# Kernel tuning notes

Measured on AMD Instinct MI355X. Metric: run time of the kernel, lower is better.

Reference implementation:

```python
import jax, jax.numpy as jnp
import numpy as np

D_MODEL = 1024
D_STATE = 64
D_CONV = 4
EXPAND = 2
HEADDIM = 64
NGROUPS = 1
D_INNER = EXPAND * D_MODEL          # 2048 (= d_ssm)
NHEADS = D_INNER // HEADDIM         # 32
CONV_DIM = D_INNER + 2 * NGROUPS * D_STATE      # 2176
D_IN_PROJ = 2 * D_INNER + 2 * NGROUPS * D_STATE + NHEADS  # 4256
BATCH, SEQLEN = 1, 1024
EPS = 1e-5


def silu(x):
    return x * jax.nn.sigmoid(x)


def _causal_dwconv(xBC, conv_w, conv_b):
    # xBC: (B, L, C); conv_w: (C, W) depthwise; causal padding W-1 on the left
    x = jnp.transpose(xBC, (0, 2, 1))  # (B, C, L)
    y = jax.lax.conv_general_dilated(
        x, conv_w[:, None, :], window_strides=(1,),
        padding=[(conv_w.shape[-1] - 1, 0)],
        feature_group_count=x.shape[1])
    return jnp.transpose(y, (0, 2, 1)) + conv_b


def _mamba_dir(u, W_in, conv_w, conv_b, dt_bias, A_log, D, norm_w, W_out):
    B, L, _ = u.shape
    H, P, G, N = NHEADS, HEADDIM, NGROUPS, D_STATE
    zxbcdt = u @ W_in.T                               # (B, L, D_IN_PROJ)
    z = zxbcdt[..., :D_INNER]
    xBC = zxbcdt[..., D_INNER:D_INNER + CONV_DIM]
    dt = zxbcdt[..., -H:]
    xBC = silu(_causal_dwconv(xBC, conv_w, conv_b))
    x = xBC[..., :D_INNER].reshape(B, L, H, P)
    Bm = xBC[..., D_INNER:D_INNER + G * N].reshape(B, L, G, N)
    Cm = xBC[..., D_INNER + G * N:].reshape(B, L, G, N)
    dt = jax.nn.softplus(dt + dt_bias)                # (B, L, H)
    A = -jnp.exp(A_log.astype(jnp.float32))           # (H,)
    rep = H // G
    Bh = jnp.repeat(Bm, rep, axis=2)                  # (B, L, H, N)
    Ch = jnp.repeat(Cm, rep, axis=2)
    dA = jnp.exp(dt * A)                              # (B, L, H)
    dtx = dt[..., None] * x                           # (B, L, H, P)

    def step(h, inp):
        dA_t, dtx_t, Bh_t, Ch_t = inp                 # (B,H), (B,H,P), (B,H,N), (B,H,N)
        h = h * dA_t[..., None, None] + jnp.einsum('bhp,bhn->bhpn', dtx_t, Bh_t)
        y = jnp.einsum('bhpn,bhn->bhp', h, Ch_t)
        return h, y

    h0 = jnp.zeros((B, H, P, N), dtype=u.dtype)
    inputs = (dA.swapaxes(0, 1), dtx.swapaxes(0, 1),
              Bh.swapaxes(0, 1), Ch.swapaxes(0, 1))
    _, ys = jax.lax.scan(step, h0, inputs)            # ys: (L, B, H, P)
    y = ys.swapaxes(0, 1) + D[None, None, :, None] * x
    y = y.reshape(B, L, D_INNER)
    # gated RMSNorm (norm_before_gate=False): norm(y * silu(z)), group = d_ssm/ngroups
    yg = y * silu(z)
    yg = yg.reshape(B, L, G, -1)
    yg = yg * jax.lax.rsqrt(jnp.mean(yg * yg, axis=-1, keepdims=True) + EPS)
    yg = yg.reshape(B, L, D_INNER) * norm_w
    return yg @ W_out.T                               # (B, L, d_model)


def _forward(u, W_in_f, W_in_b, conv_w_f, conv_b_f, conv_w_b, conv_b_b,
             dt_bias_f, dt_bias_b, A_log_f, A_log_b, D_f, D_b,
             norm_w_f, norm_w_b, W_out_f, W_out_b, W_out):
    out_f = _mamba_dir(u, W_in_f, conv_w_f, conv_b_f, dt_bias_f, A_log_f,
                       D_f, norm_w_f, W_out_f)
    ub = jnp.flip(u, axis=1)
    out_b = _mamba_dir(ub, W_in_b, conv_w_b, conv_b_b, dt_bias_b, A_log_b,
                       D_b, norm_w_b, W_out_b)
    out = silu(jnp.concatenate([out_f, jnp.flip(out_b, axis=1)], axis=-1))
    return out @ W_out.T


def setup_inputs() -> dict:
    key = jax.random.key(0)
    ks = jax.random.split(key, 20)
    s = 0.02

    def dt_init(k):
        dt = jnp.exp(jax.random.uniform(k, (NHEADS,)) *
                     (np.log(0.1) - np.log(0.001)) + np.log(0.001))
        return dt + jnp.log(-jnp.expm1(-dt))  # inverse softplus

    def a_init(k):
        return jnp.log(jax.random.uniform(k, (NHEADS,), minval=1.0, maxval=16.0))

    return {
        'u': jax.random.normal(ks[0], (BATCH, SEQLEN, D_MODEL), jnp.float32),
        'W_in_f': jax.random.normal(ks[1], (D_IN_PROJ, D_MODEL), jnp.float32) * s,
        'W_in_b': jax.random.normal(ks[2], (D_IN_PROJ, D_MODEL), jnp.float32) * s,
        'conv_w_f': jax.random.normal(ks[3], (CONV_DIM, D_CONV), jnp.float32) * 0.2,
        'conv_b_f': jnp.zeros((CONV_DIM,), jnp.float32),
        'conv_w_b': jax.random.normal(ks[4], (CONV_DIM, D_CONV), jnp.float32) * 0.2,
        'conv_b_b': jnp.zeros((CONV_DIM,), jnp.float32),
        'dt_bias_f': dt_init(ks[5]),
        'dt_bias_b': dt_init(ks[6]),
        'A_log_f': a_init(ks[7]),
        'A_log_b': a_init(ks[8]),
        'D_f': jnp.ones((NHEADS,), jnp.float32),
        'D_b': jnp.ones((NHEADS,), jnp.float32),
        'norm_w_f': jnp.ones((D_INNER,), jnp.float32),
        'norm_w_b': jnp.ones((D_INNER,), jnp.float32),
        'W_out_f': jax.random.normal(ks[9], (D_MODEL, D_INNER), jnp.float32) * s,
        'W_out_b': jax.random.normal(ks[10], (D_MODEL, D_INNER), jnp.float32) * s,
        'W_out': jax.random.normal(ks[11], (D_MODEL, 2 * D_MODEL), jnp.float32) * s,
    }


def reference(u, W_in_f, W_in_b, conv_w_f, conv_b_f, conv_w_b, conv_b_b,
              dt_bias_f, dt_bias_b, A_log_f, A_log_b, D_f, D_b,
              norm_w_f, norm_w_b, W_out_f, W_out_b, W_out):
    return _forward(u, W_in_f, W_in_b, conv_w_f, conv_b_f, conv_w_b, conv_b_b,
                    dt_bias_f, dt_bias_b, A_log_f, A_log_b, D_f, D_b,
                    norm_w_f, norm_w_b, W_out_f, W_out_b, W_out)
```

## Files before the change

### kernel.cpp

```cpp
#include <hip/hip_runtime.h>
#include <hip/hip_bf16.h>
#include <stdint.h>

#define LSEQ   1024
#define DINNER 2048
#define CONVD  2176
#define LDP    4352
#define NH     32
#define HD     64
#define NST    64
#define CHUNK  64
#define NCH    16
#define LDT    72

#define POFF_CWF  0
#define POFF_CBF  8704
#define POFF_CWB  10880
#define POFF_CBB  19584
#define POFF_DTBF 21760
#define POFF_DTBB 21792
#define POFF_ALF  21824
#define POFF_ALB  21856
#define POFF_DF   21888
#define POFF_DB   21920
#define POFF_NWF  21952
#define POFF_NWB  24000
#define PTOT      26048

#define BF16_ONES 0x3F803F80u

typedef short v8s __attribute__((ext_vector_type(8)));
typedef short v4s __attribute__((ext_vector_type(4)));
typedef float v4f __attribute__((ext_vector_type(4)));
using bf16 = __hip_bfloat16;

__device__ __forceinline__ float loadf(const void* p, size_t i, int isbf) {
    return isbf ? __bfloat162float(((const bf16*)p)[i]) : ((const float*)p)[i];
}
__device__ __forceinline__ float s2f(short s) {
    unsigned u = ((unsigned)(unsigned short)s) << 16; float f;
    __builtin_memcpy(&f, &u, 4); return f;
}
__device__ __forceinline__ short f2s(float f) {
    bf16 b = __float2bfloat16(f); short s;
    __builtin_memcpy(&s, &b, 2); return s;
}
__device__ __forceinline__ void load8(const void* p, size_t i, int isbf, float* o) {
    if (isbf) {
        v8s s = *(const v8s*)((const short*)p + i);
        #pragma unroll
        for (int e = 0; e < 8; e++) o[e] = s2f(s[e]);
    } else {
        float4 a = *(const float4*)((const float*)p + i);
        float4 b = *(const float4*)((const float*)p + i + 4);
        o[0] = a.x; o[1] = a.y; o[2] = a.z; o[3] = a.w;
        o[4] = b.x; o[5] = b.y; o[6] = b.z; o[7] = b.w;
    }
}
__device__ __forceinline__ v8s pack8(const float* o) {
    v8s r;
    #pragma unroll
    for (int e = 0; e < 8; e++) r[e] = f2s(o[e]);
    return r;
}

__device__ __forceinline__ void gload16(const bf16* g, bf16* l) {
    __builtin_amdgcn_global_load_lds(
        (const __attribute__((address_space(1))) void*)g,
        (__attribute__((address_space(3))) void*)l, 16, 0, 0);
}

template<int V> __device__ __forceinline__ void vwait() {
    if constexpr (V == 0) asm volatile("s_waitcnt vmcnt(0)" ::: "memory");
    else if constexpr (V == 3) asm volatile("s_waitcnt vmcnt(3)" ::: "memory");
    else if constexpr (V == 4) asm volatile("s_waitcnt vmcnt(4)" ::: "memory");
    else if constexpr (V == 6) asm volatile("s_waitcnt vmcnt(6)" ::: "memory");
    else if constexpr (V == 8) asm volatile("s_waitcnt vmcnt(8)" ::: "memory");
}

#define NPU  262144
#define NPW  1114112
#define NWO  786432
#define NSEG (NPU + NPW + NWO)
__global__ void prep_all(const void* __restrict__ U, const void* __restrict__ Wf, const void* __restrict__ Wb,
                         const void* __restrict__ Wof, const void* __restrict__ Wob, const void* __restrict__ Wom,
                         const void* cwf, const void* cbf, const void* cwb, const void* cbb,
                         const void* dtbf, const void* dtbb, const void* alf, const void* alb,
                         const void* df, const void* db, const void* nwf, const void* nwb,
                         bf16* __restrict__ Au, bf16* __restrict__ Wp,
                         bf16* __restrict__ Woc, bf16* __restrict__ Wo2,
                         float* __restrict__ P, int* __restrict__ flag)
{
    int idx = blockIdx.x * 256 + threadIdx.x;
    int f = (((const unsigned int*)nwf)[0] == BF16_ONES) ? 1 : 0;
    if (idx < NPU) {
        int r = idx >> 7, c8 = (idx & 127) * 8;
        int src = (r < 1024) ? r : (2047 - r);
        float o[8]; load8(U, (size_t)src * 1024 + c8, f, o);
        *(v8s*)(Au + (size_t)r * 1024 + c8) = pack8(o);
    } else if (idx < NPU + NPW) {
        int j = idx - NPU;
        int r = (j >> 7) % 4352;
        int d = j / (4352 * 128);
        int c8 = (j & 127) * 8;
        float o[8] = {0.f, 0.f, 0.f, 0.f, 0.f, 0.f, 0.f, 0.f};
        if (r < 4256) load8(d ? Wb : Wf, (size_t)r * 1024 + c8, f, o);
        *(v8s*)(Wp + (size_t)j * 8) = pack8(o);
    } else if (idx < NSEG) {
        int j = idx - NPU - NPW;
        int seg = j / 262144;
        size_t j8 = (size_t)(j % 262144) * 8;
        float o[8];
        if (seg == 0)      { load8(Wof, j8, f, o); *(v8s*)(Woc + j8) = pack8(o); }
        else if (seg == 1) { load8(Wob, j8, f, o); *(v8s*)(Woc + 1024 * 2048 + j8) = pack8(o); }
        else               { load8(Wom, j8, f, o); *(v8s*)(Wo2 + j8) = pack8(o); }
    } else if (idx < NSEG + PTOT) {
        int j = idx - NSEG;
        if (j == 0) *flag = f;
        float v;
        if      (j < POFF_CBF)  v = loadf(cwf,  j,              f);
        else if (j < POFF_CWB)  v = loadf(cbf,  j - POFF_CBF,   f);
        else if (j < POFF_CBB)  v = loadf(cwb,  j - POFF_CWB,   f);
        else if (j < POFF_DTBF) v = loadf(cbb,  j - POFF_CBB,   f);
        else if (j < POFF_DTBB) v = loadf(dtbf, j - POFF_DTBF,  f);
        else if (j < POFF_ALF)  v = loadf(dtbb, j - POFF_DTBB,  f);
        else if (j < POFF_ALB)  v = loadf(alf,  j - POFF_ALF,   f);
        else if (j < POFF_DF)   v = loadf(alb,  j - POFF_ALB,   f);
        else if (j < POFF_DB)   v = loadf(df,   j - POFF_DF,    f);
        else if (j < POFF_NWF)  v = loadf(db,   j - POFF_DB,    f);
        else if (j < POFF_NWB)  v = loadf(nwf,  j - POFF_NWF,   f);
        else                    v = loadf(nwb,  j - POFF_NWB,   f);
        P[j] = v;
    }
}

template<int BM, int BN, int BK>
__global__ __launch_bounds__(256) void gemm_bt(
    const bf16* __restrict__ A, const bf16* __restrict__ B0, const bf16* __restrict__ B1,
    int rowSplit, void* __restrict__ Cv, int M, int N, int K, const int* outFlag,
    int epi, int swzMode)
{
    constexpr int RPL = 2048 / BK;
    constexpr int AN  = BM / RPL;
    constexpr int BNN = BN / RPL;
    constexpr int LPS = AN + BNN;
    constexpr int MI  = BM / 32;
    constexpr int NJ  = BN / 32;
    constexpr int KS  = BK / 32;
    constexpr int CPR = BK / 8;
    __shared__ __align__(16) bf16 LdsA[4][BM * BK];
    __shared__ __align__(16) bf16 LdsB[4][BN * BK];
    const int tid  = threadIdx.x;
    const int lane = tid & 63;
    const int wave = tid >> 6;
    const int quad = lane >> 4, l16 = lane & 15;
    const int wrow = (wave >> 1) * (BM / 2);
    const int wcol = (wave & 1)  * (BN / 2);

    int bx = blockIdx.x, by = blockIdx.y;
    if (swzMode >= 0) {
        const int gx = gridDim.x, gy = gridDim.y;
        const int nwg = gx * gy;
        const int cpx = nwg >> 3;
        const int p   = by * gx + bx;
        const int L   = (p & 7) * cpx + (p >> 3);
        if (swzMode) { by = L % gy; bx = L / gy; }
        else         { bx = L % gx; by = L / gx; }
    }
    const int m0 = by * BM;
    const int n0 = bx * BN;
    const bf16* Bp = (m0 >= rowSplit) ? B1 : B0;
    const int mode = (outFlag && !epi) ? *outFlag : 1;

    const int r0 = tid / CPR;
    const int pc = tid % CPR;
    const int fx_w = (BK == 32) ? ((r0 >> 1) & 3) : (r0 & 7);
    const int csw = (pc ^ fx_w) * 8;
    const bf16* gA[AN];
    const bf16* gB[BNN];
    #pragma unroll
    for (int a = 0; a < AN; a++)  gA[a] = A  + (size_t)(m0 + r0 + RPL * a) * K + csw;
    #pragma unroll
    for (int q = 0; q < BNN; q++) gB[q] = Bp + (size_t)(n0 + r0 + RPL * q) * K + csw;

    v4f acc[MI][NJ];
    #pragma unroll
    for (int i = 0; i < MI; i++)
        #pragma unroll
        for (int j = 0; j < NJ; j++) acc[i][j] = (v4f){0.f, 0.f, 0.f, 0.f};

    const int nt = K / BK;

    auto STAGE = [&](int buf, int t) {
        const int k0 = t * BK;
        #pragma unroll
        for (int a = 0; a < AN; a++)
            gload16(gA[a] + k0, &LdsA[buf][a * 2048 + tid * 8]);
        #pragma unroll
        for (int q = 0; q < BNN; q++)
            gload16(gB[q] + k0, &LdsB[buf][q * 2048 + tid * 8]);
    };

    STAGE(0, 0);
    STAGE(1, 1);
    STAGE(2, 2);

    for (int t = 0; t < nt; ++t) {
        const int buf = t & 3;
        if (t < nt - 2)       vwait<2 * LPS>();
        else if (t == nt - 2) vwait<LPS>();
        else                  vwait<0>();
        __builtin_amdgcn_s_barrier();
        if (t + 3 < nt) STAGE((t + 3) & 3, t + 3);

        const bf16* as = &LdsA[buf][0];
        const bf16* bs = &LdsB[buf][0];
        #pragma unroll
        for (int ks = 0; ks < KS; ks++) {
            v8s af[MI], bfr[NJ];
            #pragma unroll
            for (int i = 0; i < MI; i++) {
                int row = wrow + i * 16 + l16;
                int fx = (BK == 32) ? ((row >> 1) & 3) : (row & 7);
                af[i] = *(const v8s*)&as[row * BK + (((ks * 4 + quad) ^ fx)) * 8];
            }
            #pragma unroll
            for (int j = 0; j < NJ; j++) {
                int row = wcol + j * 16 + l16;
                int fx = (BK == 32) ? ((row >> 1) & 3) : (row & 7);
                bfr[j] = *(const v8s*)&bs[row * BK + (((ks * 4 + quad) ^ fx)) * 8];
            }
            #pragma unroll
            for (int i = 0; i < MI; i++)
                #pragma unroll
                for (int j = 0; j < NJ; j++)
                    acc[i][j] = __builtin_amdgcn_mfma_f32_16x16x32_bf16(af[i], bfr[j], acc[i][j], 0, 0, 0);
        }
    }

    #pragma unroll
    for (int i = 0; i < MI; i++) {
        int row = m0 + wrow + i * 16 + quad * 4;
        #pragma unroll
        for (int j = 0; j < NJ; j++) {
            int col = n0 + wcol + j * 16 + l16;
            if (epi) {
                bf16* Act = (bf16*)Cv;
                #pragma unroll
                for (int r = 0; r < 4; r++) {
                    float x = acc[i][j][r];
                    float v = x / (1.f + __expf(-x));
                    int rr = row + r;
                    if (rr < 1024) Act[(size_t)rr * 2048 + col] = __float2bfloat16(v);
                    else           Act[(size_t)(2047 - rr) * 2048 + 1024 + col] = __float2bfloat16(v);
                }
            } else if (mode) {
                bf16* C = (bf16*)Cv;
                #pragma unroll
                for (int r = 0; r < 4; r++)
                    C[(size_t)(row + r) * N + col] = __float2bfloat16(acc[i][j][r]);
            } else {
                float* C = (float*)Cv;
                #pragma unroll
                for (int r = 0; r < 4; r++)
                    C[(size_t)(row + r) * N + col] = acc[i][j][r];
            }
        }
    }
}

#define NCONV (2 * LSEQ * (CONVD / 8))
#define NDT   (2 * LSEQ * NH)
__global__ void conv_dt(const bf16* __restrict__ Z, const float* __restrict__ P,
                        bf16* __restrict__ XC, float* __restrict__ DT, float* __restrict__ LDA)
{
    int idx = blockIdx.x * 256 + threadIdx.x;
    if (idx < NCONV) {
        int c8 = (idx % (CONVD / 8)) * 8;
        int l = (idx / (CONVD / 8)) % LSEQ;
        int d = idx / ((CONVD / 8) * LSEQ);
        const float* w    = P + (d ? POFF_CWB : POFF_CWF) + c8 * 4;
        const float* bias = P + (d ? POFF_CBB : POFF_CBF) + c8;
        const bf16* zbase = Z + ((size_t)(d * LSEQ + l)) * LDP + DINNER + c8;
        float s[8];
        #pragma unroll
        for (int e = 0; e < 8; e++) s[e] = bias[e];
        #pragma unroll
        for (int k = 0; k < 4; k++) {
            int ls = l - 3 + k;
            if (ls >= 0) {
                v8s zv = *(const v8s*)(zbase + (ls - l) * LDP);
                #pragma unroll
                for (int e = 0; e < 8; e++) s[e] += w[e * 4 + k] * s2f(zv[e]);
            }
        }
        float o[8];
        #pragma unroll
        for (int e = 0; e < 8; e++) o[e] = s[e] / (1.f + __expf(-s[e]));
        *(v8s*)(XC + (size_t)(d * LSEQ + l) * CONVD + c8) = pack8(o);
    } else if (idx < NCONV + NDT) {
        int j = idx - NCONV;
        int h = j & 31; int l = (j >> 5) & (LSEQ - 1); int d = j >> 15;
        float raw = s2f(((const short*)Z)[((size_t)(d * LSEQ + l)) * LDP + DINNER + CONVD + h])
                  + P[POFF_DTBF + d * 32 + h];
        float dt = (raw > 20.f) ? raw : log1pf(__expf(raw));
        float Aa = -__expf(P[POFF_ALF + d * 32 + h]);
        DT[j] = dt;
        LDA[j] = Aa * dt;
    }
}

__global__ __launch_bounds__(256) void ssd_intra(const bf16* __restrict__ XC,
                                                 const float* __restrict__ DT,
                                                 const float* __restrict__ LDA,
                                                 bf16* __restrict__ Yi, bf16* __restrict__ S,
                                                 float* __restrict__ Pdec, float* __restrict__ LSg)
{
    __shared__ __align__(16) short sB [64 * LDT];
    __shared__ __align__(16) short sBT[64 * LDT];
    __shared__ __align__(16) short sC [64 * LDT];
    __shared__ __align__(16) short sXT[64 * LDT];
    __shared__ float sls[64], sdt[64], sW[64];
    short* sGW = sC;

    int b = blockIdx.x;
    int d = b >> 9, h = (b >> 4) & 31, c = b & 15;
    int r0 = c * CHUNK;
    int t = threadIdx.x;
    const bf16* base = XC + (size_t)d * LSEQ * CONVD;

    {
        int l = t >> 2, nb = (t & 3) * 16;
        int q = t & 3;
        int cswt = (((l >> 3) ^ q) * 8) + (l & 7);
        const bf16* row = base + (size_t)(r0 + l) * CONVD;
        const short* Brow = (const short*)(row + DINNER) + nb;
        const short* Crow = (const short*)(row + DINNER + NST) + nb;
        const short* Xrow = (const short*)(row + h * HD) + nb;
        v8s b0 = *(const v8s*)Brow, b1 = *(const v8s*)(Brow + 8);
        v8s c0 = *(const v8s*)Crow, c1 = *(const v8s*)(Crow + 8);
        v8s x0 = *(const v8s*)Xrow, x1 = *(const v8s*)(Xrow + 8);
        *(v8s*)&sB[l * LDT + nb]     = b0;
        *(v8s*)&sB[l * LDT + nb + 8] = b1;
        *(v8s*)&sC[l * LDT + nb]     = c0;
        *(v8s*)&sC[l * LDT + nb + 8] = c1;
        #pragma unroll
        for (int k = 0; k < 8; k++) {
            sBT[(nb + k)     * LDT + cswt] = b0[k];
            sBT[(nb + 8 + k) * LDT + cswt] = b1[k];
            sXT[(nb + k)     * LDT + cswt] = x0[k];
            sXT[(nb + 8 + k) * LDT + cswt] = x1[k];
        }
    }
    if (t < 64) {
        size_t ofs = (size_t)d * LSEQ * NH + (size_t)(r0 + t) * NH + h;
        float v = LDA[ofs];
        float dtv = DT[ofs];
        #pragma unroll
        for (int off = 1; off < 64; off <<= 1) {
            float u = __shfl_up(v, off);
            if (t >= off) v += u;
        }
        sls[t] = v; sdt[t] = dtv;
        float ls63 = __shfl(v, 63);
        sW[t] = __expf(ls63 - v) * dtv;
        LSg[(size_t)b * 64 + t] = v;
        if (t == 63) Pdec[b] = __expf(v);
    }
    __syncthreads();

    int lane = t & 63, wave = t >> 6;
    int quad = lane >> 4, l16 = lane & 15;

    {
        v8s a0 = *(const v8s*)&sC[(wave * 16 + l16) * LDT + quad * 8];
        v8s a1 = *(const v8s*)&sC[(wave * 16 + l16) * LDT + quad * 8 + 32];
        #pragma unroll
        for (int jt = 0; jt < 4; jt++) {
            v8s b0 = *(const v8s*)&sB[(jt * 16 + l16) * LDT + quad * 8];
            v8s b1 = *(const v8s*)&sB[(jt * 16 + l16) * LDT + quad * 8 + 32];
            v4f acc = (v4f){0.f, 0.f, 0.f, 0.f};
            acc = __builtin_amdgcn_mfma_f32_16x16x32_bf16(a0, b0, acc, 0, 0, 0);
            acc = __builtin_amdgcn_mfma_f32_16x16x32_bf16(a1, b1, acc, 0, 0, 0);
            #pragma unroll
            for (int r = 0; r < 4; r++) {
                int ii = wave * 16 + quad * 4 + r;
                int jj = jt * 16 + l16;
                float wgt = (jj <= ii) ? __expf(sls[ii] - sls[jj]) * sdt[jj] : 0.f;
                sGW[ii * LDT + jj] = f2s(acc[r] * wgt);
            }
        }
    }
    __syncthreads();

    bf16* ybase = Yi + ((size_t)d * LSEQ + r0) * DINNER + h * HD;

    {
        v8s a0 = *(const v8s*)&sGW[(wave * 16 + l16) * LDT + quad * 8];
        v8s a1 = *(const v8s*)&sGW[(wave * 16 + l16) * LDT + quad * 8 + 32];
        #pragma unroll
        for (int pt = 0; pt < 4; pt++) {
            int sb = (quad ^ (pt & 3)) * 8;
            v8s b0 = *(const v8s*)&sXT[(pt * 16 + l16) * LDT + sb];
            v8s b1 = *(const v8s*)&sXT[(pt * 16 + l16) * LDT + sb + 32];
            v4f acc = (v4f){0.f, 0.f, 0.f, 0.f};
            acc = __builtin_amdgcn_mfma_f32_16x16x32_bf16(a0, b0, acc, 0, 0, 0);
            acc = __builtin_amdgcn_mfma_f32_16x16x32_bf16(a1, b1, acc, 0, 0, 0);
            #pragma unroll
            for (int r = 0; r < 4; r++) {
                int ii = wave * 16 + quad * 4 + r;
                int p  = pt * 16 + l16;
                ybase[(size_t)ii * DINNER + p] = __float2bfloat16(acc[r]);
            }
        }
    }

    {
        int sa = (quad ^ (wave & 3)) * 8;
        v8s a0r = *(const v8s*)&sXT[(wave * 16 + l16) * LDT + sa];
        v8s a1r = *(const v8s*)&sXT[(wave * 16 + l16) * LDT + sa + 32];
        v8s a0, a1;
        #pragma unroll
        for (int e = 0; e < 8; e++) {
            a0[e] = f2s(s2f(a0r[e]) * sW[quad * 8 + e]);
            a1[e] = f2s(s2f(a1r[e]) * sW[quad * 8 + 32 + e]);
        }
        short* sout = (short*)S + (size_t)b * 4096;
        #pragma unroll
        for (int nt = 0; nt < 4; nt++) {
            int sb = (quad ^ (nt & 3)) * 8;
            v8s b0 = *(const v8s*)&sBT[(nt * 16 + l16) * LDT + sb];
            v8s b1 = *(const v8s*)&sBT[(nt * 16 + l16) * LDT + sb + 32];
            v4f acc = (v4f){0.f, 0.f, 0.f, 0.f};
            acc = __builtin_amdgcn_mfma_f32_16x16x32_bf16(a0, b0, acc, 0, 0, 0);
            acc = __builtin_amdgcn_mfma_f32_16x16x32_bf16(a1, b1, acc, 0, 0, 0);
            #pragma unroll
            for (int r = 0; r < 4; r++) {
                int p = wave * 16 + quad * 4 + r;
                int n = nt * 16 + l16;
                sout[p * 64 + n] = f2s(acc[r]);
            }
        }
    }
}

__global__ __launch_bounds__(256) void scan2(bf16* __restrict__ S, const float* __restrict__ Pdec)
{
    int b = blockIdx.x;
    int off = blockIdx.y * 1024 + threadIdx.x * 4;
    short* base = (short*)S + (size_t)b * 16 * 4096 + off;
    float pc[NCH];
    #pragma unroll
    for (int c = 0; c < NCH; c++) pc[c] = Pdec[b * 16 + c];
    float h0 = 0.f, h1 = 0.f, h2 = 0.f, h3 = 0.f;
    v4s nxt = *(const v4s*)base;
    #pragma unroll
    for (int c = 0; c < NCH; c++) {
        short* so = base + (size_t)c * 4096;
        v4s sc = nxt;
        if (c + 1 < NCH) nxt = *(const v4s*)(so + 4096);
        float Pc = pc[c];
        v4s hv; hv[0] = f2s(h0); hv[1] = f2s(h1); hv[2] = f2s(h2); hv[3] = f2s(h3);
        *(v4s*)so = hv;
        h0 = h0 * Pc + s2f(sc[0]);
        h1 = h1 * Pc + s2f(sc[1]);
        h2 = h2 * Pc + s2f(sc[2]);
        h3 = h3 * Pc + s2f(sc[3]);
    }
}

__global__ __launch_bounds__(256) void ssd_inter(const bf16* __restrict__ XC,
                                                 const bf16* __restrict__ Hin,
                                                 const float* __restrict__ LSg,
                                                 bf16* __restrict__ Ye)
{
    __shared__ __align__(16) short sH [64 * LDT];
    __shared__ __align__(16) short sCk[64 * LDT];
    __shared__ float sEls[64];

    int b = blockIdx.x;
    int d = b >> 9, h = (b >> 4) & 31, c = b & 15;
    int r0 = c * CHUNK;
    int t = threadIdx.x;
    const bf16* base = XC + (size_t)d * LSEQ * CONVD;
    {
        int l = t >> 2, nb = (t & 3) * 16;
        const short* hrow = (const short*)Hin + (size_t)b * 4096 + l * 64 + nb;
        const short* crow = (const short*)(base + (size_t)(r0 + l) * CONVD + DINNER + NST) + nb;
        v8s h0 = *(const v8s*)hrow, h1 = *(const v8s*)(hrow + 8);
        v8s c0 = *(const v8s*)crow, c1 = *(const v8s*)(crow + 8);
        *(v8s*)&sH[l * LDT + nb]      = h0;
        *(v8s*)&sH[l * LDT + nb + 8]  = h1;
        *(v8s*)&sCk[l * LDT + nb]     = c0;
        *(v8s*)&sCk[l * LDT + nb + 8] = c1;
    }
    if (t < 64) sEls[t] = __expf(LSg[(size_t)b * 64 + t]);
    __syncthreads();

    int lane = t & 63, wave = t >> 6;
    int quad = lane >> 4, l16 = lane & 15;
    bf16* ybase = Ye + ((size_t)d * LSEQ + r0) * DINNER + h * HD;

    v8s a0 = *(const v8s*)&sCk[(wave * 16 + l16) * LDT + quad * 8];
    v8s a1 = *(const v8s*)&sCk[(wave * 16 + l16) * LDT + quad * 8 + 32];
    #pragma unroll
    for (int pt = 0; pt < 4; pt++) {
        v8s b0 = *(const v8s*)&sH[(pt * 16 + l16) * LDT + quad * 8];
        v8s b1 = *(const v8s*)&sH[(pt * 16 + l16) * LDT + quad * 8 + 32];
        v4f acc = (v4f){0.f, 0.f, 0.f, 0.f};
        acc = __builtin_amdgcn_mfma_f32_16x16x32_bf16(a0, b0, acc, 0, 0, 0);
        acc = __builtin_amdgcn_mfma_f32_16x16x32_bf16(a1, b1, acc, 0, 0, 0);
        #pragma unroll
        for (int r = 0; r < 4; r++) {
            int ii = wave * 16 + quad * 4 + r;
            int p  = pt * 16 + l16;
            ybase[(size_t)ii * DINNER + p] = __float2bfloat16(sEls[ii] * acc[r]);
        }
    }
}

__global__ __launch_bounds__(256) void gate_norm(const bf16* __restrict__ Yi, const bf16* __restrict__ Ye,
                                                 const bf16* __restrict__ XC,
                                                 const bf16* __restrict__ Z, const float* __restrict__ P,
                                                 bf16* __restrict__ YG)
{
    int rowi = blockIdx.x;
    int d = rowi >> 10;
    int tid = threadIdx.x;
    const bf16* yirow = Yi + (size_t)rowi * DINNER;
    const bf16* yerow = Ye + (size_t)rowi * DINNER;
    const bf16* xrow = XC + (size_t)rowi * CONVD;
    const bf16* zrow = Z + (size_t)rowi * LDP;
    const float* Dv = P + POFF_DF + d * 32;
    const float* nw = P + POFF_NWF + d * 2048;
    int j0 = tid * 8;
    float Dh = Dv[j0 >> 6];
    v8s yi8 = *(const v8s*)(yirow + j0);
    v8s ye8 = *(const v8s*)(yerow + j0);
    v8s xv8 = *(const v8s*)(xrow + j0);
    v8s zv = *(const v8s*)(zrow + j0);
    float g[8]; float ss = 0.f;
    #pragma unroll
    for (int e = 0; e < 8; e++) {
        float y = s2f(yi8[e]) + s2f(ye8[e]) + Dh * s2f(xv8[e]);
        float z = s2f(zv[e]);
        float gg = y * (z / (1.f + __expf(-z)));
        g[e] = gg; ss += gg * gg;
    }
    #pragma unroll
    for (int off = 32; off; off >>= 1) ss += __shfl_xor(ss, off);
    __shared__ float red[4];
    if ((tid & 63) == 0) red[tid >> 6] = ss;
    __syncthreads();
    float tot = red[0] + red[1] + red[2] + red[3];
    float scale = rsqrtf(tot * (1.f / 2048.f) + 1e-5f);
    float o[8];
    #pragma unroll
    for (int e = 0; e < 8; e++) o[e] = g[e] * scale * nw[j0 + e];
    *(v8s*)(YG + (size_t)rowi * DINNER + j0) = pack8(o);
}

extern "C" void kernel_launch(void* const* d_in, const int* in_sizes, int n_in,
                              void* d_out, int out_size, void* d_ws, size_t ws_size,
                              hipStream_t stream)
{
    const void* u      = d_in[0];
    const void* Winf   = d_in[1];
    const void* Winb   = d_in[2];
    const void* convwf = d_in[3];
    const void* convbf = d_in[4];
    const void* convwb = d_in[5];
    const void* convbb = d_in[6];
    const void* dtbf   = d_in[7];
    const void* dtbb   = d_in[8];
    const void* Alf    = d_in[9];
    const void* Alb    = d_in[10];
    const void* Dfv    = d_in[11];
    const void* Dbv    = d_in[12];
    const void* nwf    = d_in[13];
    const void* nwb    = d_in[14];
    const void* Woutf  = d_in[15];
    const void* Woutb  = d_in[16];
    const void* Wout   = d_in[17];

    char* w = (char*)d_ws;
    int*   flag = (int*)w;   w += 256;
    bf16*  Au   = (bf16*)w;  w += (size_t)2048 * 1024 * 2;
    bf16*  Wp   = (bf16*)w;  w += (size_t)2 * 4352 * 1024 * 2;
    bf16*  Woc  = (bf16*)w;
    bf16*  Act  = (bf16*)w;  w += (size_t)2 * 1024 * 2048 * 2;
    bf16*  Wo2  = (bf16*)w;  w += (size_t)1024 * 2048 * 2;
    float* P    = (float*)w; w += 104448;
    bf16*  Zb   = (bf16*)w;  w += (size_t)2048 * 4352 * 2;
    bf16*  XC   = (bf16*)w;  w += (size_t)2048 * 2176 * 2;
    float* DT   = (float*)w; w += (size_t)2048 * 32 * 4;
    float* LDA  = (float*)w; w += (size_t)2048 * 32 * 4;
    bf16*  YG   = (bf16*)w;  w += (size_t)2048 * 2048 * 2;
    bf16*  S    = (bf16*)w;  w += (size_t)2 * 32 * 16 * 64 * 64 * 2;
    float* Pdec = (float*)w; w += 4096;
    float* LSg  = (float*)w; w += (size_t)2 * 32 * 16 * 64 * 4;
    bf16*  Yi   = (bf16*)w;  w += (size_t)2048 * 2048 * 2;
    bf16*  Ye   = (bf16*)w;  w += (size_t)2048 * 2048 * 2;
    if ((size_t)(w - (char*)d_ws) > ws_size) return;

    prep_all<<<(NSEG + PTOT + 255) / 256, 256, 0, stream>>>(
        u, Winf, Winb, Woutf, Woutb, Wout,
        convwf, convbf, convwb, convbb, dtbf, dtbb, Alf, Alb, Dfv, Dbv, nwf, nwb,
        Au, Wp, Woc, Wo2, P, flag);

    dim3 g1(4352 / 64, 2048 / 128);
    gemm_bt<128, 64, 32><<<g1, 256, 0, stream>>>(Au, Wp, Wp + (size_t)4352 * 1024, 1024,
                                                 Zb, 2048, 4352, 1024, nullptr, 0, 1);

    conv_dt<<<(NCONV + NDT + 255) / 256, 256, 0, stream>>>(Zb, P, XC, DT, LDA);

    ssd_intra<<<1024, 256, 0, stream>>>(XC, DT, LDA, Yi, S, Pdec, LSg);
    scan2<<<dim3(64, 4), 256, 0, stream>>>(S, Pdec);
    ssd_inter<<<1024, 256, 0, stream>>>(XC, S, LSg, Ye);

    gate_norm<<<2048, 256, 0, stream>>>(Yi, Ye, XC, Zb, P, YG);

    dim3 g2(1024 / 64, 2048 / 64);
    gemm_bt<64, 64, 64><<<g2, 256, 0, stream>>>(YG, Woc, Woc + (size_t)1024 * 2048, 1024,
                                                Act, 2048, 1024, 2048, nullptr, 1, -1);

    dim3 g3(1024 / 64, 1024 / 64);
    gemm_bt<64, 64, 64><<<g3, 256, 0, stream>>>(Act, Wo2, Wo2, 1 << 30,
                                                d_out, 1024, 1024, 2048, flag, 0, -1);
}
```

Baseline: 276.9 us.

## Fuse inter-chunk state scan into ssd_inter and register-block causal conv over time

Removes the separate scan2 launch: each ssd_inter block now recomputes its incoming chunk state by scanning the previous chunk states from S with the decay factors. This saves a kernel launch and the write-back of scanned states, but adds redundant, quadratic-in-chunk-count reads of S across blocks. Separately, the causal depthwise conv now has each thread handle 8 consecutive timesteps, keeping the sliding window in registers, so each input row is loaded once instead of four times.

```diff
diff --git a/kernel.cpp b/kernel.cpp
--- a/kernel.cpp
+++ b/kernel.cpp
@@ -269,37 +269,52 @@
     }
 }
 
-#define NCONV (2 * LSEQ * (CONVD / 8))
+#define NCV2  (2 * 128 * (CONVD / 8))
 #define NDT   (2 * LSEQ * NH)
 __global__ void conv_dt(const bf16* __restrict__ Z, const float* __restrict__ P,
                         bf16* __restrict__ XC, float* __restrict__ DT, float* __restrict__ LDA)
 {
     int idx = blockIdx.x * 256 + threadIdx.x;
-    if (idx < NCONV) {
-        int c8 = (idx % (CONVD / 8)) * 8;
-        int l = (idx / (CONVD / 8)) % LSEQ;
-        int d = idx / ((CONVD / 8) * LSEQ);
+    if (idx < NCV2) {
+        int c8g = idx % (CONVD / 8);
+        int lb  = (idx / (CONVD / 8)) & 127;
+        int d   = idx / ((CONVD / 8) * 128);
+        int c8  = c8g * 8;
+        int l0  = lb * 8;
         const float* w    = P + (d ? POFF_CWB : POFF_CWF) + c8 * 4;
         const float* bias = P + (d ? POFF_CBB : POFF_CBF) + c8;
-        const bf16* zbase = Z + ((size_t)(d * LSEQ + l)) * LDP + DINNER + c8;
-        float s[8];
-        #pragma unroll
-        for (int e = 0; e < 8; e++) s[e] = bias[e];
-        #pragma unroll
-        for (int k = 0; k < 4; k++) {
-            int ls = l - 3 + k;
-            if (ls >= 0) {
-                v8s zv = *(const v8s*)(zbase + (ls - l) * LDP);
-                #pragma unroll
-                for (int e = 0; e < 8; e++) s[e] += w[e * 4 + k] * s2f(zv[e]);
-            }
-        }
-        float o[8];
-        #pragma unroll
-        for (int e = 0; e < 8; e++) o[e] = s[e] / (1.f + __expf(-s[e]));
-        *(v8s*)(XC + (size_t)(d * LSEQ + l) * CONVD + c8) = pack8(o);
-    } else if (idx < NCONV + NDT) {
-        int j = idx - NCONV;
+        const short* zcol = (const short*)Z + ((size_t)d * LSEQ) * LDP + DINNER + c8;
+        float wv[32], bv[8];
+        #pragma unroll
+        for (int e = 0; e < 8; e++) {
+            bv[e] = bias[e];
+            #pragma unroll
+            for (int k = 0; k < 4; k++) wv[e * 4 + k] = w[e * 4 + k];
+        }
+        v8s zm3, zm2, zm1;
+        #pragma unroll
+        for (int e = 0; e < 8; e++) { zm3[e] = 0; zm2[e] = 0; zm1[e] = 0; }
+        if (l0 > 0) {
+            zm3 = *(const v8s*)(zcol + (size_t)(l0 - 3) * LDP);
+            zm2 = *(const v8s*)(zcol + (size_t)(l0 - 2) * LDP);
+            zm1 = *(const v8s*)(zcol + (size_t)(l0 - 1) * LDP);
+        }
+        #pragma unroll
+        for (int i = 0; i < 8; i++) {
+            int l = l0 + i;
+            v8s z0 = *(const v8s*)(zcol + (size_t)l * LDP);
+            float o[8];
+            #pragma unroll
+            for (int e = 0; e < 8; e++) {
+                float s = bv[e] + wv[e * 4 + 0] * s2f(zm3[e]) + wv[e * 4 + 1] * s2f(zm2[e])
+                        + wv[e * 4 + 2] * s2f(zm1[e]) + wv[e * 4 + 3] * s2f(z0[e]);
+                o[e] = s / (1.f + __expf(-s));
+            }
+            *(v8s*)(XC + (size_t)(d * LSEQ + l) * CONVD + c8) = pack8(o);
+            zm3 = zm2; zm2 = zm1; zm1 = z0;
+        }
+    } else if (idx < NCV2 + NDT) {
+        int j = idx - NCV2;
         int h = j & 31; int l = (j >> 5) & (LSEQ - 1); int d = j >> 15;
         float raw = s2f(((const short*)Z)[((size_t)(d * LSEQ + l)) * LDP + DINNER + CONVD + h])
                   + P[POFF_DTBF + d * 32 + h];
@@ -444,33 +459,9 @@
     }
 }
 
-__global__ __launch_bounds__(256) void scan2(bf16* __restrict__ S, const float* __restrict__ Pdec)
-{
-    int b = blockIdx.x;
-    int off = blockIdx.y * 1024 + threadIdx.x * 4;
-    short* base = (short*)S + (size_t)b * 16 * 4096 + off;
-    float pc[NCH];
-    #pragma unroll
-    for (int c = 0; c < NCH; c++) pc[c] = Pdec[b * 16 + c];
-    float h0 = 0.f, h1 = 0.f, h2 = 0.f, h3 = 0.f;
-    v4s nxt = *(const v4s*)base;
-    #pragma unroll
-    for (int c = 0; c < NCH; c++) {
-        short* so = base + (size_t)c * 4096;
-        v4s sc = nxt;
-        if (c + 1 < NCH) nxt = *(const v4s*)(so + 4096);
-        float Pc = pc[c];
-        v4s hv; hv[0] = f2s(h0); hv[1] = f2s(h1); hv[2] = f2s(h2); hv[3] = f2s(h3);
-        *(v4s*)so = hv;
-        h0 = h0 * Pc + s2f(sc[0]);
-        h1 = h1 * Pc + s2f(sc[1]);
-        h2 = h2 * Pc + s2f(sc[2]);
-        h3 = h3 * Pc + s2f(sc[3]);
-    }
-}
-
 __global__ __launch_bounds__(256) void ssd_inter(const bf16* __restrict__ XC,
-                                                 const bf16* __restrict__ Hin,
+                                                 const bf16* __restrict__ S,
+                                                 const float* __restrict__ Pdec,
                                                  const float* __restrict__ LSg,
                                                  bf16* __restrict__ Ye)
 {
@@ -485,14 +476,37 @@
     const bf16* base = XC + (size_t)d * LSEQ * CONVD;
     {
         int l = t >> 2, nb = (t & 3) * 16;
-        const short* hrow = (const short*)Hin + (size_t)b * 4096 + l * 64 + nb;
         const short* crow = (const short*)(base + (size_t)(r0 + l) * CONVD + DINNER + NST) + nb;
-        v8s h0 = *(const v8s*)hrow, h1 = *(const v8s*)(hrow + 8);
         v8s c0 = *(const v8s*)crow, c1 = *(const v8s*)(crow + 8);
-        *(v8s*)&sH[l * LDT + nb]      = h0;
-        *(v8s*)&sH[l * LDT + nb + 8]  = h1;
         *(v8s*)&sCk[l * LDT + nb]     = c0;
         *(v8s*)&sCk[l * LDT + nb + 8] = c1;
+        float H[16];
+        #pragma unroll
+        for (int e = 0; e < 16; e++) H[e] = 0.f;
+        if (c > 0) {
+            const short* Sb = (const short*)S + ((size_t)(d * 32 + h) * 16) * 4096 + l * 64 + nb;
+            const float* Pp = Pdec + (d * 32 + h) * 16;
+            v8s s0 = *(const v8s*)Sb;
+            v8s s1 = *(const v8s*)(Sb + 8);
+            for (int j = 0; j < c; ++j) {
+                v8s n0 = s0, n1 = s1;
+                if (j + 1 < c) {
+                    s0 = *(const v8s*)(Sb + (size_t)(j + 1) * 4096);
+                    s1 = *(const v8s*)(Sb + (size_t)(j + 1) * 4096 + 8);
+                }
+                float Pj = Pp[j];
+                #pragma unroll
+                for (int e = 0; e < 8; e++) {
+                    H[e]     = H[e]     * Pj + s2f(n0[e]);
+                    H[8 + e] = H[8 + e] * Pj + s2f(n1[e]);
+                }
+            }
+        }
+        v8s h0, h1;
+        #pragma unroll
+        for (int e = 0; e < 8; e++) { h0[e] = f2s(H[e]); h1[e] = f2s(H[8 + e]); }
+        *(v8s*)&sH[l * LDT + nb]     = h0;
+        *(v8s*)&sH[l * LDT + nb + 8] = h1;
     }
     if (t < 64) sEls[t] = __expf(LSg[(size_t)b * 64 + t]);
     __syncthreads();
@@ -612,11 +626,10 @@
     gemm_bt<128, 64, 32><<<g1, 256, 0, stream>>>(Au, Wp, Wp + (size_t)4352 * 1024, 1024,
                                                  Zb, 2048, 4352, 1024, nullptr, 0, 1);
 
-    conv_dt<<<(NCONV + NDT + 255) / 256, 256, 0, stream>>>(Zb, P, XC, DT, LDA);
+    conv_dt<<<(NCV2 + NDT + 255) / 256, 256, 0, stream>>>(Zb, P, XC, DT, LDA);
 
     ssd_intra<<<1024, 256, 0, stream>>>(XC, DT, LDA, Yi, S, Pdec, LSg);
-    scan2<<<dim3(64, 4), 256, 0, stream>>>(S, Pdec);
-    ssd_inter<<<1024, 256, 0, stream>>>(XC, S, LSg, Ye);
+    ssd_inter<<<1024, 256, 0, stream>>>(XC, S, Pdec, LSg, Ye);
 
     gate_norm<<<2048, 256, 0, stream>>>(Yi, Ye, XC, Zb, P, YG);
 
```

New measurement: 252.8 us, median of 2. 8.7% less time.
